# Kernel tuning notes

Hardware: AMD Instinct MI355X
Metric: run time of the kernel (lower is better)

The kernel has to match this reference:

```python
import jax, jax.numpy as jnp
import numpy as np

B, N, K, H = 8, 2048, 30, 128
SCALE = 30.0
EPS = 1e-5


def _gelu(x):
    return jax.nn.gelu(x, approximate=False)


def _lin(x, w, b):
    return x @ w.T + b


def _ln(x, g, b):
    m = x.mean(-1, keepdims=True)
    v = ((x - m) ** 2).mean(-1, keepdims=True)
    return g * (x - m) * jax.lax.rsqrt(v + EPS) + b


def _gather_nodes(h_V, E_idx):
    # h_V: [B,N,H], E_idx: [B,N,K] -> [B,N,K,H]
    b_idx = jnp.arange(h_V.shape[0])[:, None, None]
    return h_V[b_idx, E_idx]


def setup_inputs() -> dict:
    key = jax.random.key(0)
    ks = jax.random.split(key, 16)
    p = 0.02
    inp = {
        'h_V': jax.random.normal(ks[0], (B, N, H), jnp.float32),
        'h_E': jax.random.normal(ks[1], (B, N, K, H), jnp.float32),
        'E_idx': jax.random.randint(ks[2], (B, N, K), 0, N, jnp.int32),
        'mask_V': jnp.ones((B, N), jnp.float32),
        'mask_attend': jnp.ones((B, N, K), jnp.float32),
        # node message MLP (3H -> H -> H -> H)
        'W1_w': jax.random.normal(ks[3], (H, 3 * H), jnp.float32) * p,
        'W1_b': jnp.zeros((H,), jnp.float32),
        'W2_w': jax.random.normal(ks[4], (H, H), jnp.float32) * p,
        'W2_b': jnp.zeros((H,), jnp.float32),
        'W3_w': jax.random.normal(ks[5], (H, H), jnp.float32) * p,
        'W3_b': jnp.zeros((H,), jnp.float32),
        # edge message MLP (3H -> H -> H -> H)
        'W11_w': jax.random.normal(ks[6], (H, 3 * H), jnp.float32) * p,
        'W11_b': jnp.zeros((H,), jnp.float32),
        'W12_w': jax.random.normal(ks[7], (H, H), jnp.float32) * p,
        'W12_b': jnp.zeros((H,), jnp.float32),
        'W13_w': jax.random.normal(ks[8], (H, H), jnp.float32) * p,
        'W13_b': jnp.zeros((H,), jnp.float32),
        # layer norms
        'n1_g': jnp.ones((H,), jnp.float32), 'n1_b': jnp.zeros((H,), jnp.float32),
        'n2_g': jnp.ones((H,), jnp.float32), 'n2_b': jnp.zeros((H,), jnp.float32),
        'n3_g': jnp.ones((H,), jnp.float32), 'n3_b': jnp.zeros((H,), jnp.float32),
        # position-wise FFN (H -> 4H -> H)
        'din_w': jax.random.normal(ks[9], (4 * H, H), jnp.float32) * p,
        'din_b': jnp.zeros((4 * H,), jnp.float32),
        'dout_w': jax.random.normal(ks[10], (H, 4 * H), jnp.float32) * p,
        'dout_b': jnp.zeros((H,), jnp.float32),
    }
    return inp


def reference(h_V, h_E, E_idx, mask_V, mask_attend,
              W1_w, W1_b, W2_w, W2_b, W3_w, W3_b,
              W11_w, W11_b, W12_w, W12_b, W13_w, W13_b,
              n1_g, n1_b, n2_g, n2_b, n3_g, n3_b,
              din_w, din_b, dout_w, dout_b):
    k = h_E.shape[-2]
    # --- node update ---
    h_nbr = _gather_nodes(h_V, E_idx)                       # [B,N,K,H]
    h_V_exp = jnp.broadcast_to(h_V[:, :, None, :], h_nbr.shape)
    h_EV = jnp.concatenate([h_V_exp, h_nbr, h_E], axis=-1)  # [B,N,K,3H]
    h_message = _lin(_gelu(_lin(_gelu(_lin(h_EV, W1_w, W1_b)), W2_w, W2_b)), W3_w, W3_b)
    h_message = mask_attend[..., None] * h_message
    dh = jnp.sum(h_message, axis=-2) / SCALE
    h_V = _ln(h_V + dh, n1_g, n1_b)
    dh = _lin(_gelu(_lin(h_V, din_w, din_b)), dout_w, dout_b)
    h_V = _ln(h_V + dh, n2_g, n2_b)
    h_V = mask_V[..., None] * h_V
    # --- edge update ---
    h_nbr = _gather_nodes(h_V, E_idx)
    h_V_exp = jnp.broadcast_to(h_V[:, :, None, :], h_nbr.shape)
    h_EV = jnp.concatenate([h_V_exp, h_nbr, h_E], axis=-1)
    h_message = _lin(_gelu(_lin(_gelu(_lin(h_EV, W11_w, W11_b)), W12_w, W12_b)), W13_w, W13_b)
    h_E = _ln(h_E + h_message, n3_g, n3_b)
    return (h_V, h_E)
```

## Files before the change

### kernel.cpp

```cpp
#include <hip/hip_runtime.h>

#define B_ 8
#define N_ 2048
#define K_ 30
#define H_ 128
#define LDA 136
#define EPS_ 1e-5f

typedef __attribute__((ext_vector_type(8))) short short8;
typedef __attribute__((ext_vector_type(4))) float f32x4;

__device__ inline unsigned short f2bf(float f) {
  union { float f; unsigned u; } v; v.f = f;
  unsigned r = v.u + 0x7fffu + ((v.u >> 16) & 1u);
  return (unsigned short)(r >> 16);
}

__device__ inline float bf2f(unsigned short h) {
  union { unsigned u; float f; } v; v.u = ((unsigned)h) << 16; return v.f;
}

__device__ inline float gelu_t(float x) {
  const float p = x * x;
  const float z = x * (1.5957691216057308f + 0.07135481627f * p);
  const float e = exp2f(z * -1.4426950408889634f);
  return x / (1.0f + e);
}

__device__ inline short8 pack8(float4 a, float4 b) {
  short8 o;
  o[0] = (short)f2bf(a.x); o[1] = (short)f2bf(a.y); o[2] = (short)f2bf(a.z); o[3] = (short)f2bf(a.w);
  o[4] = (short)f2bf(b.x); o[5] = (short)f2bf(b.y); o[6] = (short)f2bf(b.z); o[7] = (short)f2bf(b.w);
  return o;
}

template<int LDW, int NN>
__device__ inline void gemm64(const unsigned short* __restrict__ sA,
                              const unsigned short* __restrict__ W,
                              int lane, int cb, f32x4 (&acc)[4][NN]) {
  const int rl = lane & 15;
  const int klo = (lane >> 4) << 3;
#pragma unroll
  for (int ks = 0; ks < 4; ++ks) {
    short8 a[4];
#pragma unroll
    for (int m = 0; m < 4; ++m)
      a[m] = *(const short8*)(sA + (m * 16 + rl) * LDA + ks * 32 + klo);
#pragma unroll
    for (int n = 0; n < NN; ++n) {
      const short8 b8 = *(const short8*)(W + (size_t)(cb + n * 16 + rl) * LDW + ks * 32 + klo);
#pragma unroll
      for (int m = 0; m < 4; ++m)
        acc[m][n] = __builtin_amdgcn_mfma_f32_16x16x32_bf16(a[m], b8, acc[m][n], 0, 0, 0);
    }
  }
}

#define ZERO2(A) \
  _Pragma("unroll") for (int m_ = 0; m_ < 4; ++m_) { A[m_][0] = (f32x4){0,0,0,0}; A[m_][1] = (f32x4){0,0,0,0}; }

__global__ __launch_bounds__(256) void prep(const float* __restrict__ w1, const float* __restrict__ w2,
                                            const float* __restrict__ w3, const float* __restrict__ w11,
                                            const float* __restrict__ w12, const float* __restrict__ w13,
                                            const float* __restrict__ din, const float* __restrict__ dout,
                                            unsigned short* __restrict__ dst) {
  const int i = blockIdx.x * 256 + threadIdx.x;
  const float* s; int off;
  if (i < 49152)       { s = w1;  off = 0; }
  else if (i < 65536)  { s = w2;  off = 49152; }
  else if (i < 81920)  { s = w3;  off = 65536; }
  else if (i < 131072) { s = w11; off = 81920; }
  else if (i < 147456) { s = w12; off = 131072; }
  else if (i < 163840) { s = w13; off = 147456; }
  else if (i < 229376) { s = din; off = 163840; }
  else                 { s = dout; off = 229376; }
  dst[i] = f2bf(s[i - off]);
}

template<bool F32SRC, bool SPLIT>
__global__ __launch_bounds__(256) void preY(const void* __restrict__ Xv,
                                            const unsigned short* __restrict__ Wbase,
                                            unsigned short* __restrict__ Yc,
                                            unsigned short* __restrict__ Yn) {
  __shared__ __align__(16) unsigned short sA[64 * LDA];
  const int tid = threadIdx.x;
  const int lane = tid & 63;
  const int w = tid >> 6;
  const int rows = blockIdx.x << 6;
  const int rl = lane & 15;
  const int h4 = (lane >> 4) << 2;

  if (F32SRC) {
    const float* X = (const float*)Xv;
    for (int t = tid; t < 1024; t += 256) {
      const int r = t >> 4, seg = t & 15;
      const float* src = X + (((size_t)(rows + r)) << 7) + seg * 8;
      *(short8*)(sA + r * LDA + seg * 8) = pack8(*(const float4*)src, *(const float4*)(src + 4));
    }
  } else {
    const unsigned short* X = (const unsigned short*)Xv;
    for (int t = tid; t < 1024; t += 256) {
      const int r = t >> 4, seg = t & 15;
      *(short8*)(sA + r * LDA + seg * 8) =
          *(const short8*)(X + (((size_t)(rows + r)) << 7) + seg * 8);
    }
  }
  __syncthreads();

  const int half = w >> 1;
  const int cb = (w & 1) * 64;
  f32x4 acc[4][4];
#pragma unroll
  for (int m = 0; m < 4; ++m)
#pragma unroll
    for (int n = 0; n < 4; ++n) acc[m][n] = (f32x4){0, 0, 0, 0};
  gemm64<384, 4>(sA, Wbase + half * 128, lane, cb, acc);

  unsigned short* Y = half ? Yn : Yc;
  const int stride = SPLIT ? 128 : 256;
  const int coff = SPLIT ? 0 : half * 128;
#pragma unroll
  for (int n = 0; n < 4; ++n) {
    const int col = coff + cb + n * 16 + rl;
#pragma unroll
    for (int m = 0; m < 4; ++m)
#pragma unroll
      for (int i = 0; i < 4; ++i)
        Y[(size_t)(rows + m * 16 + h4 + i) * stride + col] = f2bf(acc[m][n][i]);
  }
}

__global__ __launch_bounds__(256, 4) void k1(
    const float* __restrict__ hV, const float* __restrict__ hE,
    const int* __restrict__ Eidx, const float* __restrict__ mattend,
    const unsigned short* __restrict__ wc, const unsigned short* __restrict__ Y1,
    const float* __restrict__ W1b, const float* __restrict__ W2b,
    const float* __restrict__ W3b, const float* __restrict__ n1g,
    const float* __restrict__ n1b, unsigned short* __restrict__ hV1b,
    float* __restrict__ outE) {
  __shared__ __align__(16) unsigned short sE[64 * LDA];
  __shared__ __align__(16) unsigned short sG[64 * LDA];
  __shared__ unsigned short sYc[2 * 128];
  __shared__ float sMask[64];
  __shared__ float sRed[2][128];

  const int tid = threadIdx.x;
  const int lane = tid & 63;
  const int w = tid >> 6;
  const int rl = lane & 15;
  const int h4 = (lane >> 4) << 2;
  const int bid = (blockIdx.x & 7) * 1024 + (blockIdx.x >> 3);
  const int v0 = bid << 1;
  const int b = v0 >> 11;
  const int n0 = v0 & (N_ - 1);
  const int bBase = b * N_;

  const unsigned short* W1c = wc;
  const unsigned short* W2c = wc + 49152;
  const unsigned short* W3c = wc + 65536;

  for (int t = tid; t < 1024; t += 256) {
    const int r = t >> 4, seg = t & 15;
    const int g = r >> 5, kk = r & 31;
    const int kc = kk < K_ ? kk : K_ - 1;
    const size_t e = (size_t)(bBase + n0 + g) * K_ + kc;
    const float* src = hE + (e << 7) + seg * 8;
    const short8 o = pack8(*(const float4*)src, *(const float4*)(src + 4));
    *(short8*)(sE + r * LDA + seg * 8) = o;
    if (kk < K_)
      *(short8*)((unsigned short*)(outE + (e << 7)) + 128 + seg * 8) = o;
  }
  for (int t = tid; t < 1024; t += 256) {
    const int r = t >> 4, seg = t & 15;
    const int g = r >> 5;
    int kk = r & 31; if (kk >= K_) kk = K_ - 1;
    const int j = Eidx[(bBase + n0 + g) * K_ + kk];
    *(short8*)(sG + r * LDA + seg * 8) =
        *(const short8*)(Y1 + (size_t)(bBase + j) * 256 + 128 + seg * 8);
  }
  {
    const int g = tid >> 7, c = tid & 127;
    sYc[g * 128 + c] = Y1[(size_t)(bBase + n0 + g) * 256 + c];
  }
  if (tid < 64) {
    const int g = tid >> 5, kk = tid & 31;
    sMask[tid] = (kk < K_) ? mattend[(bBase + n0 + g) * K_ + kk] : 0.f;
  }
  __syncthreads();

  f32x4 acc[4][2];
  ZERO2(acc)
  gemm64<384, 2>(sE, W1c + 256, lane, w * 32, acc);

#pragma unroll
  for (int n = 0; n < 2; ++n) {
    const int f = w * 32 + n * 16 + rl;
    const float bb = W1b[f];
#pragma unroll
    for (int m = 0; m < 4; ++m)
#pragma unroll
      for (int i = 0; i < 4; ++i) {
        const int e = m * 16 + h4 + i;
        const float x = acc[m][n][i] + bb + bf2f(sYc[(e >> 5) * 128 + f]) + bf2f(sG[e * LDA + f]);
        sG[e * LDA + f] = f2bf(gelu_t(x));
      }
  }
  __syncthreads();

  f32x4 acc2[4][2];
  ZERO2(acc2)
  gemm64<128, 2>(sG, W2c, lane, w * 32, acc2);
  __syncthreads();
#pragma unroll
  for (int n = 0; n < 2; ++n) {
    const int f = w * 32 + n * 16 + rl;
    const float bb = W2b[f];
#pragma unroll
    for (int m = 0; m < 4; ++m)
#pragma unroll
      for (int i = 0; i < 4; ++i) {
        const int e = m * 16 + h4 + i;
        sG[e * LDA + f] = f2bf(gelu_t(acc2[m][n][i] + bb));
      }
  }
  __syncthreads();

  f32x4 acc3[4][2];
  ZERO2(acc3)
  gemm64<128, 2>(sG, W3c, lane, w * 32, acc3);

#pragma unroll
  for (int n = 0; n < 2; ++n) {
    const int f = w * 32 + n * 16 + rl;
    const float bb = W3b[f];
#pragma unroll
    for (int g = 0; g < 2; ++g) {
      float s = 0.f;
#pragma unroll
      for (int mm = 0; mm < 2; ++mm) {
        const int m = g * 2 + mm;
#pragma unroll
        for (int i = 0; i < 4; ++i) {
          const int e = m * 16 + h4 + i;
          s += (acc3[m][n][i] + bb) * sMask[e];
        }
      }
      s += __shfl_xor(s, 16);
      s += __shfl_xor(s, 32);
      if (lane < 16) sRed[g][f] = s;
    }
  }
  __syncthreads();

  if (w < 2) {
    const size_t base = ((size_t)(bBase + n0 + w)) << 7;
    const float x0 = hV[base + lane] + sRed[w][lane] * (1.0f / 30.0f);
    const float x1 = hV[base + 64 + lane] + sRed[w][64 + lane] * (1.0f / 30.0f);
    float s = x0 + x1;
#pragma unroll
    for (int o = 1; o < 64; o <<= 1) s += __shfl_xor(s, o);
    const float mean = s * (1.0f / 128.0f);
    const float d0 = x0 - mean, d1 = x1 - mean;
    float vs = d0 * d0 + d1 * d1;
#pragma unroll
    for (int o = 1; o < 64; o <<= 1) vs += __shfl_xor(vs, o);
    const float inv = rsqrtf(vs * (1.0f / 128.0f) + EPS_);
    hV1b[base + lane] = f2bf(n1g[lane] * (d0 * inv) + n1b[lane]);
    hV1b[base + 64 + lane] = f2bf(n1g[64 + lane] * (d1 * inv) + n1b[64 + lane]);
  }
}

__global__ __launch_bounds__(256) void k2(
    const unsigned short* __restrict__ hV1b, const unsigned short* __restrict__ wc,
    const float* __restrict__ dinb, const float* __restrict__ doutb,
    const float* __restrict__ n2g, const float* __restrict__ n2b,
    const float* __restrict__ maskV, float* __restrict__ outV,
    unsigned short* __restrict__ hV2c) {
  __shared__ __align__(16) unsigned short sT[64 * LDA];
  __shared__ float sStat[64][2][4];

  const int tid = threadIdx.x;
  const int lane = tid & 63;
  const int w = tid >> 6;
  const int rowbase = blockIdx.x << 6;
  const int rl = lane & 15;
  const int klo = (lane >> 4) << 3;

  const unsigned short* dinc = wc + 163840;
  const unsigned short* doutc = wc + 229376;

  short8 a[4][4];
#pragma unroll
  for (int ks = 0; ks < 4; ++ks)
#pragma unroll
    for (int m = 0; m < 4; ++m)
      a[ks][m] = *(const short8*)(hV1b + (((size_t)(rowbase + m * 16 + rl)) << 7) + ks * 32 + klo);

  f32x4 acc2[4][2];
  ZERO2(acc2)

  for (int c = 0; c < 4; ++c) {
    f32x4 acc1[4][2];
    ZERO2(acc1)
#pragma unroll
    for (int ks = 0; ks < 4; ++ks)
#pragma unroll
      for (int n = 0; n < 2; ++n) {
        const short8 b8 = *(const short8*)(dinc + (size_t)(c * 128 + w * 32 + n * 16 + rl) * 128 + ks * 32 + klo);
#pragma unroll
        for (int m = 0; m < 4; ++m)
          acc1[m][n] = __builtin_amdgcn_mfma_f32_16x16x32_bf16(a[ks][m], b8, acc1[m][n], 0, 0, 0);
      }
    __syncthreads();
#pragma unroll
    for (int n = 0; n < 2; ++n) {
      const int col = w * 32 + n * 16 + rl;
      const float bb = dinb[c * 128 + col];
#pragma unroll
      for (int m = 0; m < 4; ++m)
#pragma unroll
        for (int i = 0; i < 4; ++i)
          sT[(m * 16 + ((lane >> 4) << 2) + i) * LDA + col] = f2bf(gelu_t(acc1[m][n][i] + bb));
    }
    __syncthreads();
#pragma unroll
    for (int ks = 0; ks < 4; ++ks) {
      short8 a2[4];
#pragma unroll
      for (int m = 0; m < 4; ++m)
        a2[m] = *(const short8*)(sT + (m * 16 + rl) * LDA + ks * 32 + klo);
#pragma unroll
      for (int n = 0; n < 2; ++n) {
        const short8 b8 = *(const short8*)(doutc + (size_t)(w * 32 + n * 16 + rl) * 512 + c * 128 + ks * 32 + klo);
#pragma unroll
        for (int m = 0; m < 4; ++m)
          acc2[m][n] = __builtin_amdgcn_mfma_f32_16x16x32_bf16(a2[m], b8, acc2[m][n], 0, 0, 0);
      }
    }
  }

  float gc[2], bc[2], wb[2];
#pragma unroll
  for (int n = 0; n < 2; ++n) {
    const int col = w * 32 + n * 16 + rl;
    gc[n] = n2g[col]; bc[n] = n2b[col]; wb[n] = doutb[col];
  }
#pragma unroll
  for (int m = 0; m < 4; ++m) {
#pragma unroll
    for (int i = 0; i < 4; ++i) {
      const int row = m * 16 + ((lane >> 4) << 2) + i;
      const unsigned short* rr = hV1b + (((size_t)(rowbase + row)) << 7) + w * 32 + rl;
      float s = 0.f, ss = 0.f;
#pragma unroll
      for (int n = 0; n < 2; ++n) {
        float x = acc2[m][n][i] + wb[n] + bf2f(rr[n * 16]);
        acc2[m][n][i] = x;
        s += x; ss += x * x;
      }
#pragma unroll
      for (int o = 1; o <= 8; o <<= 1) { s += __shfl_xor(s, o); ss += __shfl_xor(ss, o); }
      if (rl == 0) { sStat[row][0][w] = s; sStat[row][1][w] = ss; }
    }
  }
  __syncthreads();
#pragma unroll
  for (int m = 0; m < 4; ++m) {
#pragma unroll
    for (int i = 0; i < 4; ++i) {
      const int row = m * 16 + ((lane >> 4) << 2) + i;
      const int grow = rowbase + row;
      const float sum = sStat[row][0][0] + sStat[row][0][1] + sStat[row][0][2] + sStat[row][0][3];
      const float ssq = sStat[row][1][0] + sStat[row][1][1] + sStat[row][1][2] + sStat[row][1][3];
      const float mean = sum * (1.0f / 128.0f);
      const float inv = rsqrtf(ssq * (1.0f / 128.0f) - mean * mean + EPS_);
      const float mv = maskV[grow];
      float* dst = outV + (((size_t)grow) << 7) + w * 32 + rl;
      unsigned short* dstc = hV2c + (((size_t)grow) << 7) + w * 32 + rl;
#pragma unroll
      for (int n = 0; n < 2; ++n) {
        const float y = (gc[n] * (acc2[m][n][i] - mean) * inv + bc[n]) * mv;
        dst[n * 16] = y;
        dstc[n * 16] = f2bf(y);
      }
    }
  }
}

__global__ __launch_bounds__(256, 4) void k3(
    const float* __restrict__ hE_unused, const int* __restrict__ Eidx,
    const unsigned short* __restrict__ wc,
    const unsigned short* __restrict__ Y2c, const unsigned short* __restrict__ Y2n,
    const float* __restrict__ W11b, const float* __restrict__ W12b,
    const float* __restrict__ W13b, const float* __restrict__ n3g,
    const float* __restrict__ n3b, float* __restrict__ outE) {
  __shared__ __align__(16) unsigned short sE[64 * LDA];
  __shared__ __align__(16) unsigned short sG[64 * LDA];
  __shared__ unsigned short sYc[2 * 128];
  __shared__ float sStat[64][2][4];

  const int tid = threadIdx.x;
  const int lane = tid & 63;
  const int w = tid >> 6;
  const int rl = lane & 15;
  const int h4 = (lane >> 4) << 2;
  const int bid = (blockIdx.x & 7) * 1024 + (blockIdx.x >> 3);
  const int v0 = bid << 1;
  const int b = v0 >> 11;
  const int n0 = v0 & (N_ - 1);
  const int bBase = b * N_;

  const unsigned short* W11c = wc + 81920;
  const unsigned short* W12c = wc + 131072;
  const unsigned short* W13c = wc + 147456;

  for (int t = tid; t < 1024; t += 256) {
    const int r = t >> 4, seg = t & 15;
    const int g = r >> 5;
    int kk = r & 31; if (kk >= K_) kk = K_ - 1;
    const size_t e = (size_t)(bBase + n0 + g) * K_ + kk;
    *(short8*)(sE + r * LDA + seg * 8) =
        *(const short8*)((const unsigned short*)(outE + (e << 7)) + 128 + seg * 8);
  }
  for (int t = tid; t < 1024; t += 256) {
    const int r = t >> 4, seg = t & 15;
    const int g = r >> 5;
    int kk = r & 31; if (kk >= K_) kk = K_ - 1;
    const int j = Eidx[(bBase + n0 + g) * K_ + kk];
    *(short8*)(sG + r * LDA + seg * 8) =
        *(const short8*)(Y2n + (size_t)(bBase + j) * 128 + seg * 8);
  }
  {
    const int g = tid >> 7, c = tid & 127;
    sYc[g * 128 + c] = Y2c[(size_t)(bBase + n0 + g) * 128 + c];
  }
  __syncthreads();

  f32x4 acc[4][2];
  ZERO2(acc)
  gemm64<384, 2>(sE, W11c + 256, lane, w * 32, acc);

#pragma unroll
  for (int n = 0; n < 2; ++n) {
    const int f = w * 32 + n * 16 + rl;
    const float bb = W11b[f];
#pragma unroll
    for (int m = 0; m < 4; ++m)
#pragma unroll
      for (int i = 0; i < 4; ++i) {
        const int e = m * 16 + h4 + i;
        const float x = acc[m][n][i] + bb + bf2f(sYc[(e >> 5) * 128 + f]) + bf2f(sG[e * LDA + f]);
        sG[e * LDA + f] = f2bf(gelu_t(x));
      }
  }
  __syncthreads();

  f32x4 acc2[4][2];
  ZERO2(acc2)
  gemm64<128, 2>(sG, W12c, lane, w * 32, acc2);
  __syncthreads();
#pragma unroll
  for (int n = 0; n < 2; ++n) {
    const int f = w * 32 + n * 16 + rl;
    const float bb = W12b[f];
#pragma unroll
    for (int m = 0; m < 4; ++m)
#pragma unroll
      for (int i = 0; i < 4; ++i) {
        const int e = m * 16 + h4 + i;
        sG[e * LDA + f] = f2bf(gelu_t(acc2[m][n][i] + bb));
      }
  }
  __syncthreads();

  f32x4 acc3[4][2];
  ZERO2(acc3)
  gemm64<128, 2>(sG, W13c, lane, w * 32, acc3);

  float gc[2], bc[2], wb[2];
#pragma unroll
  for (int n = 0; n < 2; ++n) {
    const int f = w * 32 + n * 16 + rl;
    gc[n] = n3g[f]; bc[n] = n3b[f]; wb[n] = W13b[f];
  }
#pragma unroll
  for (int m = 0; m < 4; ++m)
#pragma unroll
    for (int i = 0; i < 4; ++i) {
      const int e = m * 16 + h4 + i;
      float s = 0.f, ss = 0.f;
#pragma unroll
      for (int n = 0; n < 2; ++n) {
        const int f = w * 32 + n * 16 + rl;
        const float x = acc3[m][n][i] + wb[n] + bf2f(sE[e * LDA + f]);
        acc3[m][n][i] = x;
        s += x; ss += x * x;
      }
#pragma unroll
      for (int o = 1; o <= 8; o <<= 1) { s += __shfl_xor(s, o); ss += __shfl_xor(ss, o); }
      if (rl == 0) { sStat[e][0][w] = s; sStat[e][1][w] = ss; }
    }
  __syncthreads();
#pragma unroll
  for (int m = 0; m < 4; ++m)
#pragma unroll
    for (int i = 0; i < 4; ++i) {
      const int e = m * 16 + h4 + i;
      const int g = e >> 5, kk = e & 31;
      if (kk >= K_) continue;
      const float sum = sStat[e][0][0] + sStat[e][0][1] + sStat[e][0][2] + sStat[e][0][3];
      const float ssq = sStat[e][1][0] + sStat[e][1][1] + sStat[e][1][2] + sStat[e][1][3];
      const float mean = sum * (1.0f / 128.0f);
      const float inv = rsqrtf(ssq * (1.0f / 128.0f) - mean * mean + EPS_);
      float* dst = outE + (((size_t)((bBase + n0 + g) * K_ + kk)) << 7) + w * 32 + rl;
#pragma unroll
      for (int n = 0; n < 2; ++n)
        dst[n * 16] = gc[n] * (acc3[m][n][i] - mean) * inv + bc[n];
    }
}

extern "C" void kernel_launch(void* const* d_in, const int* in_sizes, int n_in,
                              void* d_out, int out_size, void* d_ws, size_t ws_size,
                              hipStream_t stream) {
  const float* hV = (const float*)d_in[0];
  const float* hE = (const float*)d_in[1];
  const int* Eidx = (const int*)d_in[2];
  const float* maskV = (const float*)d_in[3];
  const float* mattend = (const float*)d_in[4];
  const float* W1w = (const float*)d_in[5];   const float* W1b = (const float*)d_in[6];
  const float* W2w = (const float*)d_in[7];   const float* W2b = (const float*)d_in[8];
  const float* W3w = (const float*)d_in[9];   const float* W3b = (const float*)d_in[10];
  const float* W11w = (const float*)d_in[11]; const float* W11b = (const float*)d_in[12];
  const float* W12w = (const float*)d_in[13]; const float* W12b = (const float*)d_in[14];
  const float* W13w = (const float*)d_in[15]; const float* W13b = (const float*)d_in[16];
  const float* n1g = (const float*)d_in[17];  const float* n1b = (const float*)d_in[18];
  const float* n2g = (const float*)d_in[19];  const float* n2b = (const float*)d_in[20];
  const float* n3g = (const float*)d_in[21];  const float* n3b = (const float*)d_in[22];
  const float* dinw = (const float*)d_in[23]; const float* dinb = (const float*)d_in[24];
  const float* doutw = (const float*)d_in[25]; const float* doutb = (const float*)d_in[26];

  unsigned short* wc   = (unsigned short*)d_ws;
  unsigned short* R1   = wc + 294912;
  unsigned short* R2   = R1 + 4194304;
  unsigned short* Y1   = R1;
  unsigned short* hV1b = R2;
  unsigned short* hV2c = R1;
  unsigned short* Y2c  = R1 + 2097152;
  unsigned short* Y2n  = R2;

  float* outV = (float*)d_out;
  float* outE = outV + (size_t)B_ * N_ * H_;

  prep<<<1152, 256, 0, stream>>>(W1w, W2w, W3w, W11w, W12w, W13w, dinw, doutw, wc);
  preY<true, false><<<256, 256, 0, stream>>>(hV, wc, Y1, Y1);
  k1<<<8192, 256, 0, stream>>>(hV, hE, Eidx, mattend, wc, Y1,
                               W1b, W2b, W3b, n1g, n1b, hV1b, outE);
  k2<<<256, 256, 0, stream>>>(hV1b, wc, dinb, doutb, n2g, n2b, maskV, outV, hV2c);
  preY<false, true><<<256, 256, 0, stream>>>(hV2c, wc + 81920, Y2c, Y2n);
  k3<<<8192, 256, 0, stream>>>(hE, Eidx, wc, Y2c, Y2n,
                               W11b, W12b, W13b, n3g, n3b, outE);
}
```

Baseline: 466.4 us.

## Transpose MFMA operands in k1 and k2, vectorize epilogues, shrink k2 tiles

k1 now computes the transposed GEMM, with weights as the A operand and edges as B, so each lane holds four consecutive features. This lets the bias, GELU and bf16 conversion epilogues use vector loads, packed bf16 converts and 8-byte LDS stores. The k1 message reduction over neighbours now goes through a float LDS scratch buffer instead of shuffles. k2 is retiled to 16 rows per block across four times as many blocks, also with transposed MFMA and vectorized LayerNorm output, and GELU uses a fast reciprocal in place of a divide. The risks are extra LDS traffic and an added barrier in k1, plus less weight reuse per k2 block.

```diff
diff --git a/kernel.cpp b/kernel.cpp
--- a/kernel.cpp
+++ b/kernel.cpp
@@ -5,6 +5,7 @@
 #define K_ 30
 #define H_ 128
 #define LDA 136
+#define LDM 132
 #define EPS_ 1e-5f
 
 typedef __attribute__((ext_vector_type(8))) short short8;
@@ -20,11 +21,17 @@
   union { unsigned u; float f; } v; v.u = ((unsigned)h) << 16; return v.f;
 }
 
+__device__ inline unsigned pkbf(float lo, float hi) {
+  unsigned r;
+  asm("v_cvt_pk_bf16_f32 %0, %1, %2" : "=v"(r) : "v"(lo), "v"(hi));
+  return r;
+}
+
 __device__ inline float gelu_t(float x) {
   const float p = x * x;
   const float z = x * (1.5957691216057308f + 0.07135481627f * p);
   const float e = exp2f(z * -1.4426950408889634f);
-  return x / (1.0f + e);
+  return x * __builtin_amdgcn_rcpf(1.0f + e);
 }
 
 __device__ inline short8 pack8(float4 a, float4 b) {
@@ -33,6 +40,30 @@
   o[4] = (short)f2bf(b.x); o[5] = (short)f2bf(b.y); o[6] = (short)f2bf(b.z); o[7] = (short)f2bf(b.w);
   return o;
 }
+
+template<int LDW>
+__device__ inline void gemmT(const unsigned short* __restrict__ sA,
+                             const unsigned short* __restrict__ W,
+                             int lane, int cb, f32x4 (&acc)[4][2]) {
+  const int rl = lane & 15;
+  const int klo = (lane >> 4) << 3;
+#pragma unroll
+  for (int ks = 0; ks < 4; ++ks) {
+    short8 wf[2];
+#pragma unroll
+    for (int fn = 0; fn < 2; ++fn)
+      wf[fn] = *(const short8*)(W + (size_t)(cb + fn * 16 + rl) * LDW + ks * 32 + klo);
+#pragma unroll
+    for (int et = 0; et < 4; ++et) {
+      const short8 ef = *(const short8*)(sA + (et * 16 + rl) * LDA + ks * 32 + klo);
+      acc[et][0] = __builtin_amdgcn_mfma_f32_16x16x32_bf16(wf[0], ef, acc[et][0], 0, 0, 0);
+      acc[et][1] = __builtin_amdgcn_mfma_f32_16x16x32_bf16(wf[1], ef, acc[et][1], 0, 0, 0);
+    }
+  }
+}
+
+#define ZERO42(A) \
+  _Pragma("unroll") for (int e_ = 0; e_ < 4; ++e_) { A[e_][0] = (f32x4){0,0,0,0}; A[e_][1] = (f32x4){0,0,0,0}; }
 
 template<int LDW, int NN>
 __device__ inline void gemm64(const unsigned short* __restrict__ sA,
@@ -55,9 +86,6 @@
     }
   }
 }
-
-#define ZERO2(A) \
-  _Pragma("unroll") for (int m_ = 0; m_ < 4; ++m_) { A[m_][0] = (f32x4){0,0,0,0}; A[m_][1] = (f32x4){0,0,0,0}; }
 
 __global__ __launch_bounds__(256) void prep(const float* __restrict__ w1, const float* __restrict__ w2,
                                             const float* __restrict__ w3, const float* __restrict__ w11,
@@ -138,11 +166,13 @@
     const float* __restrict__ W3b, const float* __restrict__ n1g,
     const float* __restrict__ n1b, unsigned short* __restrict__ hV1b,
     float* __restrict__ outE) {
-  __shared__ __align__(16) unsigned short sE[64 * LDA];
-  __shared__ __align__(16) unsigned short sG[64 * LDA];
-  __shared__ unsigned short sYc[2 * 128];
+  __shared__ __align__(16) unsigned short sBuf[2 * 64 * LDA];
+  __shared__ __align__(16) unsigned short sYc[2 * 128];
   __shared__ float sMask[64];
   __shared__ float sRed[2][128];
+  unsigned short* sE = sBuf;
+  unsigned short* sG = sBuf + 64 * LDA;
+  float* sM = (float*)sBuf;
 
   const int tid = threadIdx.x;
   const int lane = tid & 63;
@@ -189,66 +219,90 @@
   __syncthreads();
 
   f32x4 acc[4][2];
-  ZERO2(acc)
-  gemm64<384, 2>(sE, W1c + 256, lane, w * 32, acc);
-
-#pragma unroll
-  for (int n = 0; n < 2; ++n) {
-    const int f = w * 32 + n * 16 + rl;
-    const float bb = W1b[f];
-#pragma unroll
-    for (int m = 0; m < 4; ++m)
-#pragma unroll
-      for (int i = 0; i < 4; ++i) {
-        const int e = m * 16 + h4 + i;
-        const float x = acc[m][n][i] + bb + bf2f(sYc[(e >> 5) * 128 + f]) + bf2f(sG[e * LDA + f]);
-        sG[e * LDA + f] = f2bf(gelu_t(x));
-      }
+  ZERO42(acc)
+  gemmT<384>(sE, W1c + 256, lane, w * 32, acc);
+
+  {
+    float4 b1v[2];
+    b1v[0] = *(const float4*)(W1b + w * 32 + h4);
+    b1v[1] = *(const float4*)(W1b + w * 32 + 16 + h4);
+#pragma unroll
+    for (int et = 0; et < 4; ++et) {
+      const int e = et * 16 + rl;
+      const int g = et >> 1;
+#pragma unroll
+      for (int fn = 0; fn < 2; ++fn) {
+        const int f0 = w * 32 + fn * 16 + h4;
+        const ushort4 yc = *(const ushort4*)(sYc + g * 128 + f0);
+        const ushort4 yn = *(const ushort4*)(sG + e * LDA + f0);
+        const float x0 = gelu_t(acc[et][fn][0] + b1v[fn].x + bf2f(yc.x) + bf2f(yn.x));
+        const float x1 = gelu_t(acc[et][fn][1] + b1v[fn].y + bf2f(yc.y) + bf2f(yn.y));
+        const float x2 = gelu_t(acc[et][fn][2] + b1v[fn].z + bf2f(yc.z) + bf2f(yn.z));
+        const float x3 = gelu_t(acc[et][fn][3] + b1v[fn].w + bf2f(yc.w) + bf2f(yn.w));
+        uint2 o; o.x = pkbf(x0, x1); o.y = pkbf(x2, x3);
+        *(uint2*)(sG + e * LDA + f0) = o;
+      }
+    }
   }
   __syncthreads();
 
   f32x4 acc2[4][2];
-  ZERO2(acc2)
-  gemm64<128, 2>(sG, W2c, lane, w * 32, acc2);
-  __syncthreads();
-#pragma unroll
-  for (int n = 0; n < 2; ++n) {
-    const int f = w * 32 + n * 16 + rl;
-    const float bb = W2b[f];
-#pragma unroll
-    for (int m = 0; m < 4; ++m)
-#pragma unroll
-      for (int i = 0; i < 4; ++i) {
-        const int e = m * 16 + h4 + i;
-        sG[e * LDA + f] = f2bf(gelu_t(acc2[m][n][i] + bb));
-      }
+  ZERO42(acc2)
+  gemmT<128>(sG, W2c, lane, w * 32, acc2);
+  __syncthreads();
+  {
+    float4 b2v[2];
+    b2v[0] = *(const float4*)(W2b + w * 32 + h4);
+    b2v[1] = *(const float4*)(W2b + w * 32 + 16 + h4);
+#pragma unroll
+    for (int et = 0; et < 4; ++et) {
+      const int e = et * 16 + rl;
+#pragma unroll
+      for (int fn = 0; fn < 2; ++fn) {
+        const int f0 = w * 32 + fn * 16 + h4;
+        const float x0 = gelu_t(acc2[et][fn][0] + b2v[fn].x);
+        const float x1 = gelu_t(acc2[et][fn][1] + b2v[fn].y);
+        const float x2 = gelu_t(acc2[et][fn][2] + b2v[fn].z);
+        const float x3 = gelu_t(acc2[et][fn][3] + b2v[fn].w);
+        uint2 o; o.x = pkbf(x0, x1); o.y = pkbf(x2, x3);
+        *(uint2*)(sG + e * LDA + f0) = o;
+      }
+    }
   }
   __syncthreads();
 
   f32x4 acc3[4][2];
-  ZERO2(acc3)
-  gemm64<128, 2>(sG, W3c, lane, w * 32, acc3);
-
-#pragma unroll
-  for (int n = 0; n < 2; ++n) {
-    const int f = w * 32 + n * 16 + rl;
-    const float bb = W3b[f];
-#pragma unroll
-    for (int g = 0; g < 2; ++g) {
-      float s = 0.f;
-#pragma unroll
-      for (int mm = 0; mm < 2; ++mm) {
-        const int m = g * 2 + mm;
-#pragma unroll
-        for (int i = 0; i < 4; ++i) {
-          const int e = m * 16 + h4 + i;
-          s += (acc3[m][n][i] + bb) * sMask[e];
-        }
-      }
-      s += __shfl_xor(s, 16);
-      s += __shfl_xor(s, 32);
-      if (lane < 16) sRed[g][f] = s;
-    }
+  ZERO42(acc3)
+  gemmT<128>(sG, W3c, lane, w * 32, acc3);
+  __syncthreads();
+
+  {
+    float4 b3v[2];
+    b3v[0] = *(const float4*)(W3b + w * 32 + h4);
+    b3v[1] = *(const float4*)(W3b + w * 32 + 16 + h4);
+#pragma unroll
+    for (int et = 0; et < 4; ++et) {
+      const int e = et * 16 + rl;
+      const float mk = sMask[e];
+#pragma unroll
+      for (int fn = 0; fn < 2; ++fn) {
+        const int f0 = w * 32 + fn * 16 + h4;
+        const float4 v = make_float4((acc3[et][fn][0] + b3v[fn].x) * mk,
+                                     (acc3[et][fn][1] + b3v[fn].y) * mk,
+                                     (acc3[et][fn][2] + b3v[fn].z) * mk,
+                                     (acc3[et][fn][3] + b3v[fn].w) * mk);
+        *(float4*)(sM + e * LDM + f0) = v;
+      }
+    }
+  }
+  __syncthreads();
+
+  {
+    const int g = tid >> 7, f = tid & 127;
+    float s = 0.f;
+#pragma unroll
+    for (int kk = 0; kk < 32; ++kk) s += sM[(g * 32 + kk) * LDM + f];
+    sRed[g][f] = s;
   }
   __syncthreads();
 
@@ -276,120 +330,114 @@
     const float* __restrict__ n2g, const float* __restrict__ n2b,
     const float* __restrict__ maskV, float* __restrict__ outV,
     unsigned short* __restrict__ hV2c) {
-  __shared__ __align__(16) unsigned short sT[64 * LDA];
-  __shared__ float sStat[64][2][4];
+  __shared__ __align__(16) unsigned short sT[16 * LDA];
+  __shared__ float sStat[16][2][4];
 
   const int tid = threadIdx.x;
   const int lane = tid & 63;
   const int w = tid >> 6;
-  const int rowbase = blockIdx.x << 6;
   const int rl = lane & 15;
+  const int h4 = (lane >> 4) << 2;
   const int klo = (lane >> 4) << 3;
+  const int rowbase = blockIdx.x << 4;
 
   const unsigned short* dinc = wc + 163840;
   const unsigned short* doutc = wc + 229376;
 
-  short8 a[4][4];
+  short8 ef[4];
 #pragma unroll
   for (int ks = 0; ks < 4; ++ks)
-#pragma unroll
-    for (int m = 0; m < 4; ++m)
-      a[ks][m] = *(const short8*)(hV1b + (((size_t)(rowbase + m * 16 + rl)) << 7) + ks * 32 + klo);
-
-  f32x4 acc2[4][2];
-  ZERO2(acc2)
+    ef[ks] = *(const short8*)(hV1b + (((size_t)(rowbase + rl)) << 7) + ks * 32 + klo);
+
+  f32x4 acc2[2];
+  acc2[0] = (f32x4){0, 0, 0, 0}; acc2[1] = (f32x4){0, 0, 0, 0};
 
   for (int c = 0; c < 4; ++c) {
-    f32x4 acc1[4][2];
-    ZERO2(acc1)
+    f32x4 acc1[2];
+    acc1[0] = (f32x4){0, 0, 0, 0}; acc1[1] = (f32x4){0, 0, 0, 0};
 #pragma unroll
     for (int ks = 0; ks < 4; ++ks)
 #pragma unroll
-      for (int n = 0; n < 2; ++n) {
-        const short8 b8 = *(const short8*)(dinc + (size_t)(c * 128 + w * 32 + n * 16 + rl) * 128 + ks * 32 + klo);
-#pragma unroll
-        for (int m = 0; m < 4; ++m)
-          acc1[m][n] = __builtin_amdgcn_mfma_f32_16x16x32_bf16(a[ks][m], b8, acc1[m][n], 0, 0, 0);
+      for (int fn = 0; fn < 2; ++fn) {
+        const short8 wf = *(const short8*)(dinc + (size_t)(c * 128 + w * 32 + fn * 16 + rl) * 128 + ks * 32 + klo);
+        acc1[fn] = __builtin_amdgcn_mfma_f32_16x16x32_bf16(wf, ef[ks], acc1[fn], 0, 0, 0);
       }
     __syncthreads();
-#pragma unroll
-    for (int n = 0; n < 2; ++n) {
-      const int col = w * 32 + n * 16 + rl;
-      const float bb = dinb[c * 128 + col];
-#pragma unroll
-      for (int m = 0; m < 4; ++m)
-#pragma unroll
-        for (int i = 0; i < 4; ++i)
-          sT[(m * 16 + ((lane >> 4) << 2) + i) * LDA + col] = f2bf(gelu_t(acc1[m][n][i] + bb));
+    {
+      float4 db[2];
+      db[0] = *(const float4*)(dinb + c * 128 + w * 32 + h4);
+      db[1] = *(const float4*)(dinb + c * 128 + w * 32 + 16 + h4);
+#pragma unroll
+      for (int fn = 0; fn < 2; ++fn) {
+        const int f0 = w * 32 + fn * 16 + h4;
+        const float x0 = gelu_t(acc1[fn][0] + db[fn].x);
+        const float x1 = gelu_t(acc1[fn][1] + db[fn].y);
+        const float x2 = gelu_t(acc1[fn][2] + db[fn].z);
+        const float x3 = gelu_t(acc1[fn][3] + db[fn].w);
+        uint2 o; o.x = pkbf(x0, x1); o.y = pkbf(x2, x3);
+        *(uint2*)(sT + rl * LDA + f0) = o;
+      }
     }
     __syncthreads();
 #pragma unroll
     for (int ks = 0; ks < 4; ++ks) {
-      short8 a2[4];
-#pragma unroll
-      for (int m = 0; m < 4; ++m)
-        a2[m] = *(const short8*)(sT + (m * 16 + rl) * LDA + ks * 32 + klo);
-#pragma unroll
-      for (int n = 0; n < 2; ++n) {
-        const short8 b8 = *(const short8*)(doutc + (size_t)(w * 32 + n * 16 + rl) * 512 + c * 128 + ks * 32 + klo);
-#pragma unroll
-        for (int m = 0; m < 4; ++m)
-          acc2[m][n] = __builtin_amdgcn_mfma_f32_16x16x32_bf16(a2[m], b8, acc2[m][n], 0, 0, 0);
-      }
-    }
-  }
-
-  float gc[2], bc[2], wb[2];
-#pragma unroll
-  for (int n = 0; n < 2; ++n) {
-    const int col = w * 32 + n * 16 + rl;
-    gc[n] = n2g[col]; bc[n] = n2b[col]; wb[n] = doutb[col];
-  }
-#pragma unroll
-  for (int m = 0; m < 4; ++m) {
-#pragma unroll
-    for (int i = 0; i < 4; ++i) {
-      const int row = m * 16 + ((lane >> 4) << 2) + i;
-      const unsigned short* rr = hV1b + (((size_t)(rowbase + row)) << 7) + w * 32 + rl;
-      float s = 0.f, ss = 0.f;
-#pragma unroll
-      for (int n = 0; n < 2; ++n) {
-        float x = acc2[m][n][i] + wb[n] + bf2f(rr[n * 16]);
-        acc2[m][n][i] = x;
-        s += x; ss += x * x;
-      }
-#pragma unroll
-      for (int o = 1; o <= 8; o <<= 1) { s += __shfl_xor(s, o); ss += __shfl_xor(ss, o); }
-      if (rl == 0) { sStat[row][0][w] = s; sStat[row][1][w] = ss; }
-    }
-  }
-  __syncthreads();
-#pragma unroll
-  for (int m = 0; m < 4; ++m) {
-#pragma unroll
-    for (int i = 0; i < 4; ++i) {
-      const int row = m * 16 + ((lane >> 4) << 2) + i;
-      const int grow = rowbase + row;
-      const float sum = sStat[row][0][0] + sStat[row][0][1] + sStat[row][0][2] + sStat[row][0][3];
-      const float ssq = sStat[row][1][0] + sStat[row][1][1] + sStat[row][1][2] + sStat[row][1][3];
-      const float mean = sum * (1.0f / 128.0f);
-      const float inv = rsqrtf(ssq * (1.0f / 128.0f) - mean * mean + EPS_);
-      const float mv = maskV[grow];
-      float* dst = outV + (((size_t)grow) << 7) + w * 32 + rl;
-      unsigned short* dstc = hV2c + (((size_t)grow) << 7) + w * 32 + rl;
-#pragma unroll
-      for (int n = 0; n < 2; ++n) {
-        const float y = (gc[n] * (acc2[m][n][i] - mean) * inv + bc[n]) * mv;
-        dst[n * 16] = y;
-        dstc[n * 16] = f2bf(y);
-      }
+      const short8 xf = *(const short8*)(sT + rl * LDA + ks * 32 + klo);
+#pragma unroll
+      for (int fn = 0; fn < 2; ++fn) {
+        const short8 wf2 = *(const short8*)(doutc + (size_t)(w * 32 + fn * 16 + rl) * 512 + c * 128 + ks * 32 + klo);
+        acc2[fn] = __builtin_amdgcn_mfma_f32_16x16x32_bf16(wf2, xf, acc2[fn], 0, 0, 0);
+      }
+    }
+  }
+
+  const int row = rl;
+  const int grow = rowbase + row;
+  {
+    float4 wbv[2];
+    wbv[0] = *(const float4*)(doutb + w * 32 + h4);
+    wbv[1] = *(const float4*)(doutb + w * 32 + 16 + h4);
+    float s = 0.f, ss = 0.f;
+#pragma unroll
+    for (int fn = 0; fn < 2; ++fn) {
+      const int f0 = w * 32 + fn * 16 + h4;
+      const ushort4 rr = *(const ushort4*)(hV1b + (((size_t)grow) << 7) + f0);
+      const float x0 = acc2[fn][0] + wbv[fn].x + bf2f(rr.x);
+      const float x1 = acc2[fn][1] + wbv[fn].y + bf2f(rr.y);
+      const float x2 = acc2[fn][2] + wbv[fn].z + bf2f(rr.z);
+      const float x3 = acc2[fn][3] + wbv[fn].w + bf2f(rr.w);
+      acc2[fn] = (f32x4){x0, x1, x2, x3};
+      s += x0 + x1 + x2 + x3;
+      ss += x0 * x0 + x1 * x1 + x2 * x2 + x3 * x3;
+    }
+    s += __shfl_xor(s, 16); s += __shfl_xor(s, 32);
+    ss += __shfl_xor(ss, 16); ss += __shfl_xor(ss, 32);
+    if (lane < 16) { sStat[row][0][w] = s; sStat[row][1][w] = ss; }
+  }
+  __syncthreads();
+  {
+    const float sum = sStat[row][0][0] + sStat[row][0][1] + sStat[row][0][2] + sStat[row][0][3];
+    const float ssq = sStat[row][1][0] + sStat[row][1][1] + sStat[row][1][2] + sStat[row][1][3];
+    const float mean = sum * (1.0f / 128.0f);
+    const float inv = rsqrtf(ssq * (1.0f / 128.0f) - mean * mean + EPS_);
+    const float mv = maskV[grow];
+#pragma unroll
+    for (int fn = 0; fn < 2; ++fn) {
+      const int f0 = w * 32 + fn * 16 + h4;
+      const float4 gv = *(const float4*)(n2g + f0);
+      const float4 bv = *(const float4*)(n2b + f0);
+      const float y0 = (gv.x * (acc2[fn][0] - mean) * inv + bv.x) * mv;
+      const float y1 = (gv.y * (acc2[fn][1] - mean) * inv + bv.y) * mv;
+      const float y2 = (gv.z * (acc2[fn][2] - mean) * inv + bv.z) * mv;
+      const float y3 = (gv.w * (acc2[fn][3] - mean) * inv + bv.w) * mv;
+      *(float4*)(outV + (((size_t)grow) << 7) + f0) = make_float4(y0, y1, y2, y3);
+      uint2 o; o.x = pkbf(y0, y1); o.y = pkbf(y2, y3);
+      *(uint2*)(hV2c + (((size_t)grow) << 7) + f0) = o;
     }
   }
 }
 
 __global__ __launch_bounds__(256, 4) void k3(
-    const float* __restrict__ hE_unused, const int* __restrict__ Eidx,
-    const unsigned short* __restrict__ wc,
+    const int* __restrict__ Eidx, const unsigned short* __restrict__ wc,
     const unsigned short* __restrict__ Y2c, const unsigned short* __restrict__ Y2n,
     const float* __restrict__ W11b, const float* __restrict__ W12b,
     const float* __restrict__ W13b, const float* __restrict__ n3g,
@@ -437,7 +485,7 @@
   __syncthreads();
 
   f32x4 acc[4][2];
-  ZERO2(acc)
+  ZERO42(acc)
   gemm64<384, 2>(sE, W11c + 256, lane, w * 32, acc);
 
 #pragma unroll
@@ -456,7 +504,7 @@
   __syncthreads();
 
   f32x4 acc2[4][2];
-  ZERO2(acc2)
+  ZERO42(acc2)
   gemm64<128, 2>(sG, W12c, lane, w * 32, acc2);
   __syncthreads();
 #pragma unroll
@@ -474,7 +522,7 @@
   __syncthreads();
 
   f32x4 acc3[4][2];
-  ZERO2(acc3)
+  ZERO42(acc3)
   gemm64<128, 2>(sG, W13c, lane, w * 32, acc3);
 
   float gc[2], bc[2], wb[2];
@@ -555,8 +603,8 @@
   preY<true, false><<<256, 256, 0, stream>>>(hV, wc, Y1, Y1);
   k1<<<8192, 256, 0, stream>>>(hV, hE, Eidx, mattend, wc, Y1,
                                W1b, W2b, W3b, n1g, n1b, hV1b, outE);
-  k2<<<256, 256, 0, stream>>>(hV1b, wc, dinb, doutb, n2g, n2b, maskV, outV, hV2c);
+  k2<<<1024, 256, 0, stream>>>(hV1b, wc, dinb, doutb, n2g, n2b, maskV, outV, hV2c);
   preY<false, true><<<256, 256, 0, stream>>>(hV2c, wc + 81920, Y2c, Y2n);
-  k3<<<8192, 256, 0, stream>>>(hE, Eidx, wc, Y2c, Y2n,
+  k3<<<8192, 256, 0, stream>>>(Eidx, wc, Y2c, Y2n,
                                W11b, W12b, W13b, n3g, n3b, outE);
 }
```

Result: no change. 460.6 us (-1.2%).
